# Kernel optimization log

Measured on AMD Instinct MI355X. Metric: run time of the kernel, lower is better.

## Reference

```python
import jax, jax.numpy as jnp
import numpy as np

N, B, G, D = 262144, 4096, 8, 7
NODE_DIM, GLOBAL_DIM, HIDDEN = 128, 128, 64
NEG = -1000000000.0


def setup_inputs() -> dict:
    key = jax.random.key(0)
    ks = jax.random.split(key, 7)
    node_features = jax.random.normal(ks[0], (N, NODE_DIM), jnp.float32)
    global_features = jax.random.normal(ks[1], (B, GLOBAL_DIM), jnp.float32)
    group_mask_nodes = jax.random.randint(ks[2], (N,), 0, 2) == 1
    batch = jnp.sort(jax.random.randint(ks[3], (N,), 0, B)).astype(jnp.int32)
    maneuver_mask = jax.random.randint(ks[4], (B, G, D), 0, 2) == 1
    W1 = jax.random.normal(ks[5], (NODE_DIM + GLOBAL_DIM, HIDDEN), jnp.float32) * 0.0625
    b1 = jnp.zeros((HIDDEN,), jnp.float32)
    W2 = jax.random.normal(ks[6], (HIDDEN, D), jnp.float32) * 0.125
    b2 = jnp.zeros((D,), jnp.float32)
    return {"node_features": node_features, "global_features": global_features,
            "group_mask_nodes": group_mask_nodes, "batch": batch,
            "maneuver_mask": maneuver_mask, "W1": W1, "b1": b1, "W2": W2, "b2": b2}


def reference(node_features, global_features, group_mask_nodes, batch, maneuver_mask, W1, b1, W2, b2):
    # Per-batch ragged group index: g_idx[i] = (# selected rows with same batch id before i).
    sel = group_mask_nodes
    sel_i = sel.astype(jnp.int32)
    csum = jnp.cumsum(sel_i)                                   # inclusive cumsum over selected rows
    counts = jax.ops.segment_sum(sel_i, batch, num_segments=B)  # selected rows per batch
    offsets = jnp.concatenate([jnp.zeros(1, jnp.int32), jnp.cumsum(counts)[:-1].astype(jnp.int32)])
    g_idx = csum - 1 - offsets[batch]                          # valid only where sel
    valid = sel & (g_idx < G)

    # Batched tiny MLP: concat(node, global[batch]) @ W1 done as split matmul to avoid materializing concat.
    glob = global_features[batch]                              # [N, GLOBAL_DIM] gather
    h = jax.nn.relu(node_features @ W1[:NODE_DIM] + glob @ W1[NODE_DIM:] + b1)
    out = h @ W2 + b2                                          # [N, D]

    # Scatter into padded [B, G+1, D]; invalid rows routed to dummy group slot G (sliced off).
    logits = jnp.full((B, G + 1, D), NEG, dtype=out.dtype)
    b_s = jnp.where(valid, batch, 0)
    g_s = jnp.where(valid, g_idx, G)
    logits = logits.at[b_s, g_s].set(out)
    logits = logits[:, :G, :]
    logits = jnp.where(maneuver_mask, logits, jnp.float32(NEG))
    return logits.reshape(B, G * D)
```

## Files before the change

### kernel.cpp

```cpp
#include <hip/hip_runtime.h>
#include <hip/hip_bf16.h>

#define G_SLOTS   8
#define D_OUT     7
#define NODE_DIM  128
#define GLOB_DIM  128
#define HIDDEN    64
#define NEG_VAL   (-1000000000.0f)
#define ROW_H     272
#define H_STRIDE  68
#define POUT_OFF  4352

typedef _Float16 half8 __attribute__((ext_vector_type(8)));
typedef float    f32x4 __attribute__((ext_vector_type(4)));

__global__ void seg_starts_kernel(const int* __restrict__ batch,
                                  int* __restrict__ starts, int N, int B) {
    int i = blockIdx.x * blockDim.x + threadIdx.x;
    if (i >= N) return;
    int b = batch[i];
    if (i == 0) {
        for (int bb = 0; bb <= b; ++bb) starts[bb] = 0;
    } else {
        int pb = batch[i - 1];
        for (int bb = pb + 1; bb <= b; ++bb) starts[bb] = i;
    }
    if (i == N - 1) {
        for (int bb = b + 1; bb <= B; ++bb) starts[bb] = N;
    }
}

__global__ __launch_bounds__(256) void fused_mlp_kernel(
        const float* __restrict__ node,
        const float* __restrict__ glob,
        const int* __restrict__ sel,
        const int* __restrict__ starts,
        const int* __restrict__ mmask,
        const float* __restrict__ W1,
        const float* __restrict__ b1,
        const float* __restrict__ W2,
        const float* __restrict__ b2,
        float* __restrict__ out) {
    __shared__ __align__(16) _Float16 xa[64 * ROW_H];
    __shared__ __align__(16) _Float16 wt[64 * ROW_H];
    __shared__ __align__(16) int starts_l[G_SLOTS + 1];
    __shared__ __align__(16) int nidxl[64];

    int t = threadIdx.x;
    int b0 = (int)blockIdx.x * 8;
    int slot0 = (int)blockIdx.x * 64;

    if (t < 9) starts_l[t] = starts[b0 + t];

    {
        int n = t & 63, ko8 = (t >> 6) * 8;
#pragma unroll
        for (int it = 0; it < 8; ++it) {
            int k0 = it * 32 + ko8;
            half8 hv;
#pragma unroll
            for (int j = 0; j < 8; ++j) {
                hv[j] = (_Float16)W1[(k0 + j) * HIDDEN + n];
            }
            *(half8*)&wt[n * ROW_H + k0] = hv;
        }
    }

    {
        int r = t >> 2, q = t & 3;
        const float* gsrc = glob + (size_t)(b0 + (r >> 3)) * GLOB_DIM + q * 32;
        int dst = r * ROW_H + 128 + q * 32;
#pragma unroll
        for (int jj = 0; jj < 4; ++jj) {
            half8 hv;
#pragma unroll
            for (int j = 0; j < 8; ++j) {
                hv[j] = (_Float16)gsrc[jj * 8 + j];
            }
            *(half8*)&xa[dst + jj * 8] = hv;
        }
    }
    __syncthreads();

    {
        int w = t >> 6, lane = t & 63;
        for (int bi = w * 2; bi < w * 2 + 2; ++bi) {
            int start = starts_l[bi], end = starts_l[bi + 1];
            int found = 0;
            for (int base = start; base < end && found < G_SLOTS; base += 64) {
                int i = base + lane;
                bool s = (i < end) && (sel[i] != 0);
                unsigned long long m = __ballot(s);
                if (s) {
                    int rank = found + __popcll(m & ((1ull << lane) - 1ull));
                    if (rank < G_SLOTS) nidxl[bi * G_SLOTS + rank] = i;
                }
                found += __popcll(m);
            }
            int f = found < G_SLOTS ? found : G_SLOTS;
            if (lane < G_SLOTS - f) nidxl[bi * G_SLOTS + f + lane] = -1;
        }
    }
    __syncthreads();

    {
        int r = t >> 2, q = t & 3;
        int nidx = nidxl[r];
        int dst = r * ROW_H + q * 32;
        if (nidx >= 0) {
            const float* src = node + (size_t)nidx * NODE_DIM + q * 32;
#pragma unroll
            for (int jj = 0; jj < 4; ++jj) {
                half8 hv;
#pragma unroll
                for (int j = 0; j < 8; ++j) {
                    hv[j] = (_Float16)src[jj * 8 + j];
                }
                *(half8*)&xa[dst + jj * 8] = hv;
            }
        } else {
            half8 hz;
#pragma unroll
            for (int j = 0; j < 8; ++j) hz[j] = (_Float16)0.0f;
#pragma unroll
            for (int jj = 0; jj < 4; ++jj) *(half8*)&xa[dst + jj * 8] = hz;
        }
    }
    __syncthreads();

    int w = t >> 6, lane = t & 63;
    int col = lane & 15, quad = lane >> 4;
    f32x4 acc0, acc1, acc2, acc3;
    acc0 = 0.0f; acc1 = 0.0f; acc2 = 0.0f; acc3 = 0.0f;
    {
        int nrow = w * 16 + col;
#pragma unroll
        for (int kt = 0; kt < 8; ++kt) {
            half8 bf = *(const half8*)&wt[nrow * ROW_H + kt * 32 + quad * 8];
            half8 a0 = *(const half8*)&xa[(0 * 16 + col) * ROW_H + kt * 32 + quad * 8];
            half8 a1 = *(const half8*)&xa[(1 * 16 + col) * ROW_H + kt * 32 + quad * 8];
            half8 a2 = *(const half8*)&xa[(2 * 16 + col) * ROW_H + kt * 32 + quad * 8];
            half8 a3 = *(const half8*)&xa[(3 * 16 + col) * ROW_H + kt * 32 + quad * 8];
            acc0 = __builtin_amdgcn_mfma_f32_16x16x32_f16(a0, bf, acc0, 0, 0, 0);
            acc1 = __builtin_amdgcn_mfma_f32_16x16x32_f16(a1, bf, acc1, 0, 0, 0);
            acc2 = __builtin_amdgcn_mfma_f32_16x16x32_f16(a2, bf, acc2, 0, 0, 0);
            acc3 = __builtin_amdgcn_mfma_f32_16x16x32_f16(a3, bf, acc3, 0, 0, 0);
        }
    }
    int nh = w * 16 + col;
    float b1v = b1[nh];
    __syncthreads();

    {
        float* H = (float*)wt;
#pragma unroll
        for (int reg = 0; reg < 4; ++reg) {
            int m0 = quad * 4 + reg;
            H[(m0 +  0) * H_STRIDE + nh] = fmaxf(acc0[reg] + b1v, 0.0f);
            H[(m0 + 16) * H_STRIDE + nh] = fmaxf(acc1[reg] + b1v, 0.0f);
            H[(m0 + 32) * H_STRIDE + nh] = fmaxf(acc2[reg] + b1v, 0.0f);
            H[(m0 + 48) * H_STRIDE + nh] = fmaxf(acc3[reg] + b1v, 0.0f);
        }
    }
    __syncthreads();

    {
        const float* H = (const float*)wt;
        float* pout = (float*)wt + POUT_OFF;
        int sl = t & 63;
        int partu = t >> 6;
        float p[D_OUT];
#pragma unroll
        for (int d = 0; d < D_OUT; ++d) p[d] = 0.0f;
#pragma unroll
        for (int jj = 0; jj < 4; ++jj) {
            float4 hq = *(const float4*)&H[sl * H_STRIDE + partu * 16 + jj * 4];
            float hv0 = hq.x, hv1 = hq.y, hv2 = hq.z, hv3 = hq.w;
            int n0 = partu * 16 + jj * 4;
#pragma unroll
            for (int d = 0; d < D_OUT; ++d) {
                float s = fmaf(hv0, W2[(n0 + 0) * D_OUT + d], p[d]);
                s = fmaf(hv1, W2[(n0 + 1) * D_OUT + d], s);
                s = fmaf(hv2, W2[(n0 + 2) * D_OUT + d], s);
                s = fmaf(hv3, W2[(n0 + 3) * D_OUT + d], s);
                p[d] = s;
            }
        }
#pragma unroll
        for (int d = 0; d < D_OUT; ++d) pout[partu * 448 + sl * D_OUT + d] = p[d];
    }
    __syncthreads();

    {
        const float* pout = (const float*)wt + POUT_OFF;
        for (int e = t; e < 64 * D_OUT; e += 256) {
            int sl = e / D_OUT, d = e - sl * D_OUT;
            float v = pout[e] + pout[448 + e] + pout[896 + e] + pout[1344 + e] + b2[d];
            int oidx = slot0 * D_OUT + e;
            bool ok = (nidxl[sl] >= 0) && (mmask[oidx] != 0);
            out[oidx] = ok ? v : NEG_VAL;
        }
    }
}

extern "C" void kernel_launch(void* const* d_in, const int* in_sizes, int n_in,
                              void* d_out, int out_size, void* d_ws, size_t ws_size,
                              hipStream_t stream) {
    const float* node  = (const float*)d_in[0];
    const float* glob  = (const float*)d_in[1];
    const int*   sel   = (const int*)d_in[2];
    const int*   batch = (const int*)d_in[3];
    const int*   mmask = (const int*)d_in[4];
    const float* W1    = (const float*)d_in[5];
    const float* b1    = (const float*)d_in[6];
    const float* W2    = (const float*)d_in[7];
    const float* b2    = (const float*)d_in[8];
    float* out = (float*)d_out;

    int N = in_sizes[3];
    int B = in_sizes[1] / GLOB_DIM;

    int* starts = (int*)d_ws;

    seg_starts_kernel<<<(N + 255) / 256, 256, 0, stream>>>(batch, starts, N, B);
    fused_mlp_kernel<<<(B * G_SLOTS) / 64, 256, 0, stream>>>(
        node, glob, sel, starts, mmask, W1, b1, W2, b2, out);
}
```

Before: 191.8 us.

## Fold segment-start computation into MLP kernel via binary search, trim barriers

Drops the separate seg_starts kernel. Each block now binary-searches the sorted batch array to find its nine segment boundaries, which removes a kernel launch and a full pass over batch. Two __syncthreads are also removed, where each wave only reads shared data that the same wave wrote. The mask and bias loads are moved to the kernel start so their latency overlaps the rest of the work. The cost is a short serial binary search in a few threads of every block.

```diff
diff --git a/kernel.cpp b/kernel.cpp
--- a/kernel.cpp
+++ b/kernel.cpp
@@ -1,5 +1,4 @@
 #include <hip/hip_runtime.h>
-#include <hip/hip_bf16.h>
 
 #define G_SLOTS   8
 #define D_OUT     7
@@ -14,33 +13,18 @@
 typedef _Float16 half8 __attribute__((ext_vector_type(8)));
 typedef float    f32x4 __attribute__((ext_vector_type(4)));
 
-__global__ void seg_starts_kernel(const int* __restrict__ batch,
-                                  int* __restrict__ starts, int N, int B) {
-    int i = blockIdx.x * blockDim.x + threadIdx.x;
-    if (i >= N) return;
-    int b = batch[i];
-    if (i == 0) {
-        for (int bb = 0; bb <= b; ++bb) starts[bb] = 0;
-    } else {
-        int pb = batch[i - 1];
-        for (int bb = pb + 1; bb <= b; ++bb) starts[bb] = i;
-    }
-    if (i == N - 1) {
-        for (int bb = b + 1; bb <= B; ++bb) starts[bb] = N;
-    }
-}
-
 __global__ __launch_bounds__(256) void fused_mlp_kernel(
         const float* __restrict__ node,
         const float* __restrict__ glob,
         const int* __restrict__ sel,
-        const int* __restrict__ starts,
+        const int* __restrict__ batch,
         const int* __restrict__ mmask,
         const float* __restrict__ W1,
         const float* __restrict__ b1,
         const float* __restrict__ W2,
         const float* __restrict__ b2,
-        float* __restrict__ out) {
+        float* __restrict__ out,
+        int N, int B) {
     __shared__ __align__(16) _Float16 xa[64 * ROW_H];
     __shared__ __align__(16) _Float16 wt[64 * ROW_H];
     __shared__ __align__(16) int starts_l[G_SLOTS + 1];
@@ -50,7 +34,27 @@
     int b0 = (int)blockIdx.x * 8;
     int slot0 = (int)blockIdx.x * 64;
 
-    if (t < 9) starts_l[t] = starts[b0 + t];
+    int e1 = t + 256;
+    int sl0 = t / D_OUT, d0 = t - sl0 * D_OUT;
+    int mm0 = mmask[slot0 * D_OUT + t];
+    float b2v0 = b2[d0];
+    int sl1 = 0, mm1 = 0; float b2v1 = 0.0f;
+    if (e1 < 64 * D_OUT) {
+        sl1 = e1 / D_OUT;
+        int d1 = e1 - sl1 * D_OUT;
+        mm1 = mmask[slot0 * D_OUT + e1];
+        b2v1 = b2[d1];
+    }
+
+    if (t < 9) {
+        int target = b0 + t;
+        int lo = 0, hi = N;
+        while (lo < hi) {
+            int mid = (lo + hi) >> 1;
+            if (batch[mid] < target) lo = mid + 1; else hi = mid;
+        }
+        starts_l[t] = lo;
+    }
 
     {
         int n = t & 63, ko8 = (t >> 6) * 8;
@@ -101,7 +105,6 @@
             if (lane < G_SLOTS - f) nidxl[bi * G_SLOTS + f + lane] = -1;
         }
     }
-    __syncthreads();
 
     {
         int r = t >> 2, q = t & 3;
@@ -162,7 +165,6 @@
             H[(m0 + 48) * H_STRIDE + nh] = fmaxf(acc3[reg] + b1v, 0.0f);
         }
     }
-    __syncthreads();
 
     {
         const float* H = (const float*)wt;
@@ -193,12 +195,13 @@
 
     {
         const float* pout = (const float*)wt + POUT_OFF;
-        for (int e = t; e < 64 * D_OUT; e += 256) {
-            int sl = e / D_OUT, d = e - sl * D_OUT;
-            float v = pout[e] + pout[448 + e] + pout[896 + e] + pout[1344 + e] + b2[d];
-            int oidx = slot0 * D_OUT + e;
-            bool ok = (nidxl[sl] >= 0) && (mmask[oidx] != 0);
-            out[oidx] = ok ? v : NEG_VAL;
+        float v0 = pout[t] + pout[448 + t] + pout[896 + t] + pout[1344 + t] + b2v0;
+        bool ok0 = (nidxl[sl0] >= 0) && (mm0 != 0);
+        out[slot0 * D_OUT + t] = ok0 ? v0 : NEG_VAL;
+        if (e1 < 64 * D_OUT) {
+            float v1 = pout[e1] + pout[448 + e1] + pout[896 + e1] + pout[1344 + e1] + b2v1;
+            bool ok1 = (nidxl[sl1] >= 0) && (mm1 != 0);
+            out[slot0 * D_OUT + e1] = ok1 ? v1 : NEG_VAL;
         }
     }
 }
@@ -220,9 +223,6 @@
     int N = in_sizes[3];
     int B = in_sizes[1] / GLOB_DIM;
 
-    int* starts = (int*)d_ws;
-
-    seg_starts_kernel<<<(N + 255) / 256, 256, 0, stream>>>(batch, starts, N, B);
     fused_mlp_kernel<<<(B * G_SLOTS) / 64, 256, 0, stream>>>(
-        node, glob, sel, starts, mmask, W1, b1, W2, b2, out);
+        node, glob, sel, batch, mmask, W1, b1, W2, b2, out, N, B);
 }
```

Result: no change. 190.7 us (-0.6%).
